# Kernel optimization log

Hardware: AMD Instinct MI355X
Metric: run time of the kernel (lower is better)

Reference implementation:

```python
import jax, jax.numpy as jnp
import numpy as np

D_MODEL, KAN_HIDDEN, NUM, K = 1024, 128, 3, 3  # grid_size=3, spline order k=3
GRID_RANGE = (-1.0, 1.0)


def make_grid(in_dim):
    # extended grid: num+1 interior knots padded by k steps of h on each side -> num+1+2k points
    h = (GRID_RANGE[1] - GRID_RANGE[0]) / NUM
    g = jnp.arange(-K, NUM + K + 1, dtype=jnp.float32) * h + GRID_RANGE[0]  # [num+1+2k]
    return jnp.broadcast_to(g, (in_dim, g.shape[0]))  # [in_dim, G]


def b_splines(x, grid):
    # Cox-de-Boor recursion. x: [N, D], grid: [D, G] -> basis [N, D, G-1-K]
    xg = x[:, :, None]  # [N, D, 1]
    B = ((xg >= grid[None, :, :-1]) & (xg < grid[None, :, 1:])).astype(x.dtype)
    for d in range(1, K + 1):
        left = (xg - grid[None, :, : -(d + 1)]) / (grid[:, d:-1] - grid[:, : -(d + 1)])[None]
        right = (grid[None, :, d + 1:] - xg) / (grid[:, d + 1:] - grid[:, 1:-d])[None]
        B = left * B[:, :, :-1] + right * B[:, :, 1:]
    return B  # [N, D, NUM+K]


def kan_layer(x, grid, coef, scale_base, scale_sp):
    # y[n,i,o] = scale_base[i,o]*silu(x[n,i]) + scale_sp[i,o]*sum_g B[n,i,g]*coef[i,o,g]; out = y.sum(i)
    B = b_splines(x, grid)  # [N, in, NUM+K]
    spline = jnp.einsum('nig,iog->no', B, coef * scale_sp[:, :, None])
    base = jnp.einsum('ni,io->no', jax.nn.silu(x), scale_base)
    return base + spline  # [N, out]


def setup_inputs() -> dict:
    key = jax.random.key(0)
    ks = jax.random.split(key, 7)
    s = 0.1  # small init scale for spline coefficients, matching noisy init spirit
    return {
        'x': jax.random.normal(ks[0], (4, 4096, D_MODEL), dtype=jnp.float32),
        'coef1': jax.random.normal(ks[1], (D_MODEL, KAN_HIDDEN, NUM + K), dtype=jnp.float32) * s,
        'scale_base1': jax.random.normal(ks[2], (D_MODEL, KAN_HIDDEN), dtype=jnp.float32),
        'scale_sp1': jnp.ones((D_MODEL, KAN_HIDDEN), dtype=jnp.float32),
        'coef2': jax.random.normal(ks[3], (KAN_HIDDEN, D_MODEL, NUM + K), dtype=jnp.float32) * s,
        'scale_base2': jax.random.normal(ks[4], (KAN_HIDDEN, D_MODEL), dtype=jnp.float32),
        'scale_sp2': jnp.ones((KAN_HIDDEN, D_MODEL), dtype=jnp.float32),
    }


def reference(x, coef1, scale_base1, scale_sp1, coef2, scale_base2, scale_sp2):
    b, s, d = x.shape
    xf = x.reshape(-1, d)  # [N, d_model]
    g1 = make_grid(D_MODEL)
    g2 = make_grid(KAN_HIDDEN)
    y1 = kan_layer(xf, g1, coef1, scale_base1, scale_sp1)   # [N, kan_hidden]
    y2 = kan_layer(y1, g2, coef2, scale_base2, scale_sp2)   # [N, d_model]
    return y2.reshape(b, s, d)
```

## Files before the change

### kernel.cpp

```cpp
#include <hip/hip_runtime.h>
#include <stdint.h>

typedef float f32x4 __attribute__((ext_vector_type(4)));
typedef __bf16 bf16x8 __attribute__((ext_vector_type(8)));

#define NROW 16384
#define DM   1024
#define HID  128
#define K1   8192
#define K2   1024

__device__ __forceinline__ unsigned short f2bf(float f) {
  unsigned u = __builtin_bit_cast(unsigned, f);
  u += 0x7fffu + ((u >> 16) & 1u);
  return (unsigned short)(u >> 16);
}

__device__ __forceinline__ uint32_t pkbf(float lo, float hi) {
  return (uint32_t)f2bf(lo) | ((uint32_t)f2bf(hi) << 16);
}

__device__ __forceinline__ void g2l16(const void* g, void* l) {
  __builtin_amdgcn_global_load_lds(
      (const __attribute__((address_space(1))) unsigned int*)g,
      (__attribute__((address_space(3))) unsigned int*)l, 16, 0, 0);
}

__device__ __forceinline__ bf16x8 expand8(float v) {
  const float t = (v + 3.0f) * 1.5f;
  const float cf = floorf(t);
  const float u = t - cf;
  int c = (int)cf;
  c = c < -1 ? -1 : c;
  c = c > 9 ? 9 : c;
  const float u2 = u * u, u3 = u2 * u, omu = 1.0f - u;
  const float p0 = u3 * (1.0f / 6.0f);
  const float p1 = (1.0f / 6.0f) + 0.5f * u + 0.5f * u2 - 0.5f * u3;
  const float p2 = (4.0f / 6.0f) - u2 + 0.5f * u3;
  const float p3 = omu * omu * omu * (1.0f / 6.0f);
  const uint64_t W = (uint64_t)pkbf(p3, p2) | ((uint64_t)pkbf(p1, p0) << 32);
  const int sa = (c - 2) * 16;
  const int sl = sa & 63;
  const uint64_t t1 = W << sl;
  const uint64_t t2 = (W >> (63 - sl)) >> 1;
  const uint64_t t3 = W >> ((-sa) & 63);
  const uint64_t L = sa < 0 ? t3 : (sa < 64 ? t1 : 0);
  const uint64_t H = sa < 0 ? 0  : (sa < 64 ? t2 : t1);
  const float s = v * __frcp_rn(1.0f + __expf(-v));
  const unsigned short sh = f2bf(s);
  const float shf = __builtin_bit_cast(float, (uint32_t)sh << 16);
  const unsigned short slo = f2bf(s - shf);
  const uint32_t w0 = ((uint32_t)L & 0xffff0000u) | sh;
  const uint32_t w1 = (uint32_t)(L >> 32);
  const uint32_t w2 = (uint32_t)H;
  const uint32_t w3 = ((uint32_t)(H >> 32) & 0xffffu) | ((uint32_t)slo << 16);
  union { uint4 q; bf16x8 b; } r;
  r.q = (uint4){w0, w1, w2, w3};
  return r.b;
}

__global__ void kan_prep_w1(const float* __restrict__ c1, const float* __restrict__ sb1,
                            const float* __restrict__ sp1, unsigned short* __restrict__ w1t) {
  const int t = blockIdx.x * 256 + threadIdx.x;
  const int o = t >> 10, i = t & 1023;
  const float sb = sb1[i * HID + o], sp = sp1[i * HID + o];
  const float* cf = c1 + (size_t)(i * HID + o) * 6;
  union { uint4 u; unsigned short h[8]; } r;
  const unsigned short b = f2bf(sb);
  r.h[0] = b; r.h[7] = b;
#pragma unroll
  for (int g = 0; g < 6; ++g) r.h[g + 1] = f2bf(cf[g] * sp);
  *(uint4*)(w1t + (size_t)o * K1 + i * 8) = r.u;
}

__global__ void kan_prep_w2(const float* __restrict__ c2, const float* __restrict__ sb2,
                            const float* __restrict__ sp2, unsigned short* __restrict__ w2t) {
  const int t = blockIdx.x * 256 + threadIdx.x;
  const int o = t >> 7, i = t & 127;
  const float sb = sb2[i * DM + o], sp = sp2[i * DM + o];
  const float* cf = c2 + (size_t)(i * DM + o) * 6;
  union { uint4 u; unsigned short h[8]; } r;
  const unsigned short b = f2bf(sb);
  r.h[0] = b; r.h[7] = b;
#pragma unroll
  for (int g = 0; g < 6; ++g) r.h[g + 1] = f2bf(cf[g] * sp);
  *(uint4*)(w2t + (size_t)o * K2 + i * 8) = r.u;
}

__global__ __launch_bounds__(512, 2) void kan_gemm1(
    const float* __restrict__ x, const unsigned short* __restrict__ w1t,
    float* __restrict__ yp) {
  __shared__ __align__(16) char lds[65536];
  const int tid = threadIdx.x;
  const int lane = tid & 63, w = tid >> 6;
  const int wk = w >> 2, wm = (w >> 1) & 1, wn = w & 1;
  const int mt = blockIdx.x >> 1, kh = blockIdx.x & 1;
  const int m0 = mt * 128;
  const int arow = tid >> 2, acs = (tid & 3) * 2;

  f32x4 acc[4][4];
#pragma unroll
  for (int a = 0; a < 4; ++a)
#pragma unroll
    for (int b = 0; b < 4; ++b) acc[a][b] = (f32x4){0.f, 0.f, 0.f, 0.f};

  const int bo = wn * 64 + (lane & 15);
  const int bk = wk * 32 + (lane >> 4) * 8;

  auto loadB = [&](int kt, bf16x8* bfrag) {
#pragma unroll
    for (int ni = 0; ni < 4; ++ni)
      bfrag[ni] = *(const bf16x8*)(w1t + (size_t)(bo + ni * 16) * K1 + kh * 4096 + kt * 64 + bk);
  };
  auto stageA = [&](float2 xv, int buf) {
    bf16x8 u0 = expand8(xv.x);
    bf16x8 u1 = expand8(xv.y);
    char* base = lds + buf * 16384;
    const int sw = (arow & 7) << 4;
    *(bf16x8*)(base + ((arow * 128 + acs * 16) ^ sw)) = u0;
    *(bf16x8*)(base + ((arow * 128 + acs * 16 + 16) ^ sw)) = u1;
  };

  const float* xrow = x + (size_t)(m0 + arow) * DM + kh * 512 + acs;
  bf16x8 bcur[4], bnxt[4];
  float2 xv = *(const float2*)xrow;
  loadB(0, bcur);
  stageA(xv, 0);
  xv = *(const float2*)(xrow + 8);
  __syncthreads();

  const int NT = 64;
  for (int kt = 0; kt < NT; ++kt) {
    const int cur = kt & 1;
    if (kt + 1 < NT) {
      loadB(kt + 1, bnxt);
      stageA(xv, cur ^ 1);
      if (kt + 2 < NT) xv = *(const float2*)(xrow + (kt + 2) * 8);
    }
    const char* ab = lds + cur * 16384;
    bf16x8 af[4];
#pragma unroll
    for (int mi = 0; mi < 4; ++mi) {
      const int row = wm * 64 + mi * 16 + (lane & 15);
      af[mi] = *(const bf16x8*)(ab + ((row * 128 + wk * 64 + (lane >> 4) * 16) ^ ((row & 7) << 4)));
    }
#pragma unroll
    for (int mi = 0; mi < 4; ++mi)
#pragma unroll
      for (int ni = 0; ni < 4; ++ni)
        acc[mi][ni] = __builtin_amdgcn_mfma_f32_16x16x32_bf16(af[mi], bcur[ni], acc[mi][ni], 0, 0, 0);
    __syncthreads();
#pragma unroll
    for (int ni = 0; ni < 4; ++ni) bcur[ni] = bnxt[ni];
  }

  if (wk == 1) {
    char* r = lds + (w & 3) * 16384;
#pragma unroll
    for (int mi = 0; mi < 4; ++mi)
#pragma unroll
      for (int ni = 0; ni < 4; ++ni)
        *(f32x4*)(r + (mi * 4 + ni) * 1024 + lane * 16) = acc[mi][ni];
  }
  __syncthreads();
  if (wk == 0) {
    const char* r = lds + w * 16384;
    float* yb = yp + (size_t)kh * NROW * HID;
#pragma unroll
    for (int mi = 0; mi < 4; ++mi)
#pragma unroll
      for (int ni = 0; ni < 4; ++ni) {
        f32x4 o = *(const f32x4*)(r + (mi * 4 + ni) * 1024 + lane * 16);
        o += acc[mi][ni];
        const int col = wn * 64 + ni * 16 + (lane & 15);
#pragma unroll
        for (int rr = 0; rr < 4; ++rr) {
          const int row = wm * 64 + mi * 16 + (lane >> 4) * 4 + rr;
          yb[(size_t)(m0 + row) * HID + col] = o[rr];
        }
      }
  }
}

__global__ void kan_combine(const float* __restrict__ yp, unsigned short* __restrict__ a2) {
  const size_t i = (size_t)blockIdx.x * 256 + threadIdx.x;
  const float v = yp[i] + yp[i + (size_t)NROW * HID];
  bf16x8 u = expand8(v);
  *(bf16x8*)(a2 + i * 8) = u;
}

__global__ __launch_bounds__(256, 2) void kan_gemm2(
    const unsigned short* __restrict__ a2, const unsigned short* __restrict__ w2t,
    float* __restrict__ out) {
  __shared__ __align__(16) unsigned short lds[2 * 16384];
  const int tid = threadIdx.x;
  const int lane = tid & 63, w = tid >> 6;
  const int wm = w >> 1, wn = w & 1;
  const int mt = blockIdx.x & 127, nt = blockIdx.x >> 7;
  const int m0 = mt * 128, n0 = nt * 128;

  f32x4 acc[4][4];
#pragma unroll
  for (int a = 0; a < 4; ++a)
#pragma unroll
    for (int b = 0; b < 4; ++b) acc[a][b] = (f32x4){0.f, 0.f, 0.f, 0.f};

  auto stage = [&](int kt, int buf) {
#pragma unroll
    for (int q = 0; q < 4; ++q) {
      const int r = (w * 4 + q) * 8 + (lane >> 3);
      const int slot = (lane & 7) ^ (lane >> 3);
      g2l16(a2 + (size_t)(m0 + r) * K2 + kt * 64 + slot * 8,
            (char*)lds + buf * 32768 + (w * 4 + q) * 1024);
      g2l16(w2t + (size_t)(n0 + r) * K2 + kt * 64 + slot * 8,
            (char*)lds + buf * 32768 + 16384 + (w * 4 + q) * 1024);
    }
  };

  stage(0, 0);
  __syncthreads();
  for (int kt = 0; kt < 16; ++kt) {
    const int cur = kt & 1;
    if (kt + 1 < 16) stage(kt + 1, cur ^ 1);
    const char* ab = (const char*)lds + cur * 32768;
    const char* bb = ab + 16384;
#pragma unroll
    for (int ks = 0; ks < 2; ++ks) {
      bf16x8 af[4], bfr[4];
#pragma unroll
      for (int mi = 0; mi < 4; ++mi) {
        const int row = wm * 64 + mi * 16 + (lane & 15);
        af[mi] = *(const bf16x8*)(ab + ((row * 128 + ks * 64 + (lane >> 4) * 16) ^ ((row & 7) << 4)));
      }
#pragma unroll
      for (int ni = 0; ni < 4; ++ni) {
        const int col = wn * 64 + ni * 16 + (lane & 15);
        bfr[ni] = *(const bf16x8*)(bb + ((col * 128 + ks * 64 + (lane >> 4) * 16) ^ ((col & 7) << 4)));
      }
#pragma unroll
      for (int mi = 0; mi < 4; ++mi)
#pragma unroll
        for (int ni = 0; ni < 4; ++ni)
          acc[mi][ni] = __builtin_amdgcn_mfma_f32_16x16x32_bf16(af[mi], bfr[ni], acc[mi][ni], 0, 0, 0);
    }
    __syncthreads();
  }

#pragma unroll
  for (int mi = 0; mi < 4; ++mi)
#pragma unroll
    for (int r = 0; r < 4; ++r) {
      const int row = wm * 64 + mi * 16 + (lane >> 4) * 4 + r;
#pragma unroll
      for (int ni = 0; ni < 4; ++ni) {
        const int col = wn * 64 + ni * 16 + (lane & 15);
        out[(size_t)(m0 + row) * DM + n0 + col] = acc[mi][ni][r];
      }
    }
}

extern "C" void kernel_launch(void* const* d_in, const int* in_sizes, int n_in,
                              void* d_out, int out_size, void* d_ws, size_t ws_size,
                              hipStream_t stream) {
  const float* x   = (const float*)d_in[0];
  const float* c1  = (const float*)d_in[1];
  const float* sb1 = (const float*)d_in[2];
  const float* sp1 = (const float*)d_in[3];
  const float* c2  = (const float*)d_in[4];
  const float* sb2 = (const float*)d_in[5];
  const float* sp2 = (const float*)d_in[6];
  float* out = (float*)d_out;

  unsigned short* w1t = (unsigned short*)d_ws;
  unsigned short* w2t = w1t + (size_t)HID * K1;
  unsigned short* a2  = w2t + (size_t)DM * K2;
  float*          yp  = (float*)(a2 + (size_t)NROW * K2);

  kan_prep_w1<<<512, 256, 0, stream>>>(c1, sb1, sp1, w1t);
  kan_prep_w2<<<512, 256, 0, stream>>>(c2, sb2, sp2, w2t);
  kan_gemm1<<<256, 512, 0, stream>>>(x, w1t, yp);
  kan_combine<<<NROW * HID / 256, 256, 0, stream>>>(yp, a2);
  kan_gemm2<<<(NROW / 128) * (DM / 128), 256, 0, stream>>>(a2, w2t, out);
}
```

Measured before the change: 130.5 us.

## Split GEMM1 K four ways with bf16 partials and halve its LDS footprint

GEMM1 now splits K across four blocks instead of two, giving 512 blocks and raising the occupancy target to 4 by halving LDS to 32KB. The cross-wave reduction moves to a two-round LDS exchange. Partial sums are written as bf16, which the combine kernel sums four at a time per thread. B fragments are loaded directly each iteration without double buffering. The spline and SiLU math uses FMAs and hardware conversion/rcp, and GEMM2 replaces syncthreads with explicit vmcnt waits plus raw barriers so the next tile's loads can overlap. The bf16 partial sums reduce precision in the intermediate activations, and the direct B loads may expose more global-load latency.

Result: slower. 135.7 us (+4.0%).

```diff
diff --git a/kernel.cpp b/kernel.cpp
--- a/kernel.cpp
+++ b/kernel.cpp
@@ -3,12 +3,15 @@
 
 typedef float f32x4 __attribute__((ext_vector_type(4)));
 typedef __bf16 bf16x8 __attribute__((ext_vector_type(8)));
+typedef __bf16 bf16x2 __attribute__((ext_vector_type(2)));
+typedef unsigned short ushort4v __attribute__((ext_vector_type(4)));
 
 #define NROW 16384
 #define DM   1024
 #define HID  128
 #define K1   8192
 #define K2   1024
+#define KSPLIT 4
 
 __device__ __forceinline__ unsigned short f2bf(float f) {
   unsigned u = __builtin_bit_cast(unsigned, f);
@@ -16,8 +19,11 @@
   return (unsigned short)(u >> 16);
 }
 
-__device__ __forceinline__ uint32_t pkbf(float lo, float hi) {
-  return (uint32_t)f2bf(lo) | ((uint32_t)f2bf(hi) << 16);
+__device__ __forceinline__ uint32_t pk2(float lo, float hi) {
+  bf16x2 v;
+  v[0] = (__bf16)lo;
+  v[1] = (__bf16)hi;
+  return __builtin_bit_cast(uint32_t, v);
 }
 
 __device__ __forceinline__ void g2l16(const void* g, void* l) {
@@ -35,10 +41,13 @@
   c = c > 9 ? 9 : c;
   const float u2 = u * u, u3 = u2 * u, omu = 1.0f - u;
   const float p0 = u3 * (1.0f / 6.0f);
-  const float p1 = (1.0f / 6.0f) + 0.5f * u + 0.5f * u2 - 0.5f * u3;
-  const float p2 = (4.0f / 6.0f) - u2 + 0.5f * u3;
-  const float p3 = omu * omu * omu * (1.0f / 6.0f);
-  const uint64_t W = (uint64_t)pkbf(p3, p2) | ((uint64_t)pkbf(p1, p0) << 32);
+  float p1 = __builtin_fmaf(0.5f, u, 1.0f / 6.0f);
+  p1 = __builtin_fmaf(0.5f, u2, p1);
+  p1 = __builtin_fmaf(-0.5f, u3, p1);
+  float p2 = __builtin_fmaf(0.5f, u3, 4.0f / 6.0f);
+  p2 = p2 - u2;
+  const float p3 = (omu * omu) * (omu * (1.0f / 6.0f));
+  const uint64_t W = (uint64_t)pk2(p3, p2) | ((uint64_t)pk2(p1, p0) << 32);
   const int sa = (c - 2) * 16;
   const int sl = sa & 63;
   const uint64_t t1 = W << sl;
@@ -46,14 +55,16 @@
   const uint64_t t3 = W >> ((-sa) & 63);
   const uint64_t L = sa < 0 ? t3 : (sa < 64 ? t1 : 0);
   const uint64_t H = sa < 0 ? 0  : (sa < 64 ? t2 : t1);
-  const float s = v * __frcp_rn(1.0f + __expf(-v));
-  const unsigned short sh = f2bf(s);
-  const float shf = __builtin_bit_cast(float, (uint32_t)sh << 16);
-  const unsigned short slo = f2bf(s - shf);
-  const uint32_t w0 = ((uint32_t)L & 0xffff0000u) | sh;
+  const float e = __expf(-v);
+  const float s = v * __builtin_amdgcn_rcpf(1.0f + e);
+  const uint32_t su = __builtin_bit_cast(uint32_t, s);
+  const uint32_t shf_bits = su & 0xffff0000u;
+  const float slo_f = s - __builtin_bit_cast(float, shf_bits);
+  const uint32_t slo = (uint32_t)__builtin_bit_cast(unsigned short, (__bf16)slo_f);
+  const uint32_t w0 = ((uint32_t)L & 0xffff0000u) | (shf_bits >> 16);
   const uint32_t w1 = (uint32_t)(L >> 32);
   const uint32_t w2 = (uint32_t)H;
-  const uint32_t w3 = ((uint32_t)(H >> 32) & 0xffffu) | ((uint32_t)slo << 16);
+  const uint32_t w3 = ((uint32_t)(H >> 32) & 0xffffu) | (slo << 16);
   union { uint4 q; bf16x8 b; } r;
   r.q = (uint4){w0, w1, w2, w3};
   return r.b;
@@ -87,14 +98,14 @@
   *(uint4*)(w2t + (size_t)o * K2 + i * 8) = r.u;
 }
 
-__global__ __launch_bounds__(512, 2) void kan_gemm1(
+__global__ __launch_bounds__(512, 4) void kan_gemm1(
     const float* __restrict__ x, const unsigned short* __restrict__ w1t,
-    float* __restrict__ yp) {
-  __shared__ __align__(16) char lds[65536];
+    unsigned short* __restrict__ yq) {
+  __shared__ __align__(16) char lds[32768];
   const int tid = threadIdx.x;
   const int lane = tid & 63, w = tid >> 6;
   const int wk = w >> 2, wm = (w >> 1) & 1, wn = w & 1;
-  const int mt = blockIdx.x >> 1, kh = blockIdx.x & 1;
+  const int mt = blockIdx.x >> 2, kh = blockIdx.x & 3;
   const int m0 = mt * 128;
   const int arow = tid >> 2, acs = (tid & 3) * 2;
 
@@ -105,88 +116,100 @@
     for (int b = 0; b < 4; ++b) acc[a][b] = (f32x4){0.f, 0.f, 0.f, 0.f};
 
   const int bo = wn * 64 + (lane & 15);
-  const int bk = wk * 32 + (lane >> 4) * 8;
-
-  auto loadB = [&](int kt, bf16x8* bfrag) {
-#pragma unroll
-    for (int ni = 0; ni < 4; ++ni)
-      bfrag[ni] = *(const bf16x8*)(w1t + (size_t)(bo + ni * 16) * K1 + kh * 4096 + kt * 64 + bk);
-  };
-  auto stageA = [&](float2 xv, int buf) {
-    bf16x8 u0 = expand8(xv.x);
-    bf16x8 u1 = expand8(xv.y);
-    char* base = lds + buf * 16384;
-    const int sw = (arow & 7) << 4;
-    *(bf16x8*)(base + ((arow * 128 + acs * 16) ^ sw)) = u0;
-    *(bf16x8*)(base + ((arow * 128 + acs * 16 + 16) ^ sw)) = u1;
-  };
-
-  const float* xrow = x + (size_t)(m0 + arow) * DM + kh * 512 + acs;
-  bf16x8 bcur[4], bnxt[4];
-  float2 xv = *(const float2*)xrow;
-  loadB(0, bcur);
-  stageA(xv, 0);
-  xv = *(const float2*)(xrow + 8);
+  const unsigned short* bp = w1t + (size_t)bo * K1 + kh * 2048 + wk * 32 + (lane >> 4) * 8;
+
+  const int wraw = arow * 128 + acs * 16;
+  const int wsw = (arow & 7) << 4;
+  char* wa0 = lds + (wraw ^ wsw);
+  char* wa1 = lds + ((wraw + 16) ^ wsw);
+  const char* ra[4];
+#pragma unroll
+  for (int mi = 0; mi < 4; ++mi) {
+    const int row = wm * 64 + mi * 16 + (lane & 15);
+    ra[mi] = lds + ((row * 128 + wk * 64 + (lane >> 4) * 16) ^ ((row & 7) << 4));
+  }
+  const float* xrow = x + (size_t)(m0 + arow) * DM + kh * 256 + acs;
+
+  bf16x8 b[4], af[4];
+  const int NT = 32;
+
+  {
+    float2 xv0 = *(const float2*)xrow;
+    *(bf16x8*)wa0 = expand8(xv0.x);
+    *(bf16x8*)wa1 = expand8(xv0.y);
+  }
+  float2 xv = *(const float2*)(xrow + 8);
   __syncthreads();
 
-  const int NT = 64;
   for (int kt = 0; kt < NT; ++kt) {
     const int cur = kt & 1;
+#pragma unroll
+    for (int ni = 0; ni < 4; ++ni)
+      b[ni] = *(const bf16x8*)(bp + (size_t)ni * 16 * K1 + kt * 64);
     if (kt + 1 < NT) {
-      loadB(kt + 1, bnxt);
-      stageA(xv, cur ^ 1);
-      if (kt + 2 < NT) xv = *(const float2*)(xrow + (kt + 2) * 8);
-    }
-    const char* ab = lds + cur * 16384;
-    bf16x8 af[4];
-#pragma unroll
-    for (int mi = 0; mi < 4; ++mi) {
-      const int row = wm * 64 + mi * 16 + (lane & 15);
-      af[mi] = *(const bf16x8*)(ab + ((row * 128 + wk * 64 + (lane >> 4) * 16) ^ ((row & 7) << 4)));
+      const int nb = (cur ^ 1) * 16384;
+      *(bf16x8*)(wa0 + nb) = expand8(xv.x);
+      *(bf16x8*)(wa1 + nb) = expand8(xv.y);
+      xv = *(const float2*)(xrow + ((kt + 2 < NT) ? kt + 2 : NT - 1) * 8);
     }
 #pragma unroll
     for (int mi = 0; mi < 4; ++mi)
+      af[mi] = *(const bf16x8*)(ra[mi] + cur * 16384);
+#pragma unroll
+    for (int mi = 0; mi < 4; ++mi)
 #pragma unroll
       for (int ni = 0; ni < 4; ++ni)
-        acc[mi][ni] = __builtin_amdgcn_mfma_f32_16x16x32_bf16(af[mi], bcur[ni], acc[mi][ni], 0, 0, 0);
+        acc[mi][ni] = __builtin_amdgcn_mfma_f32_16x16x32_bf16(af[mi], b[ni], acc[mi][ni], 0, 0, 0);
     __syncthreads();
-#pragma unroll
-    for (int ni = 0; ni < 4; ++ni) bcur[ni] = bnxt[ni];
-  }
-
-  if (wk == 1) {
-    char* r = lds + (w & 3) * 16384;
-#pragma unroll
-    for (int mi = 0; mi < 4; ++mi)
-#pragma unroll
-      for (int ni = 0; ni < 4; ++ni)
-        *(f32x4*)(r + (mi * 4 + ni) * 1024 + lane * 16) = acc[mi][ni];
-  }
-  __syncthreads();
-  if (wk == 0) {
-    const char* r = lds + w * 16384;
-    float* yb = yp + (size_t)kh * NROW * HID;
-#pragma unroll
-    for (int mi = 0; mi < 4; ++mi)
-#pragma unroll
-      for (int ni = 0; ni < 4; ++ni) {
-        f32x4 o = *(const f32x4*)(r + (mi * 4 + ni) * 1024 + lane * 16);
-        o += acc[mi][ni];
-        const int col = wn * 64 + ni * 16 + (lane & 15);
-#pragma unroll
-        for (int rr = 0; rr < 4; ++rr) {
-          const int row = wm * 64 + mi * 16 + (lane >> 4) * 4 + rr;
-          yb[(size_t)(m0 + row) * HID + col] = o[rr];
+  }
+
+  unsigned short* yb = yq + (size_t)kh * NROW * HID;
+#pragma unroll
+  for (int rnd = 0; rnd < 2; ++rnd) {
+    const int src0 = 4 + rnd * 2;
+    if (w == src0 || w == src0 + 1) {
+      char* r = lds + (w - src0) * 16384;
+#pragma unroll
+      for (int mi = 0; mi < 4; ++mi)
+#pragma unroll
+        for (int ni = 0; ni < 4; ++ni)
+          *(f32x4*)(r + (mi * 4 + ni) * 1024 + lane * 16) = acc[mi][ni];
+    }
+    __syncthreads();
+    const int snk0 = rnd * 2;
+    if (w == snk0 || w == snk0 + 1) {
+      const char* r = lds + (w - snk0) * 16384;
+#pragma unroll
+      for (int mi = 0; mi < 4; ++mi)
+#pragma unroll
+        for (int ni = 0; ni < 4; ++ni) {
+          f32x4 o = *(const f32x4*)(r + (mi * 4 + ni) * 1024 + lane * 16);
+          o += acc[mi][ni];
+          const int col = wn * 64 + ni * 16 + (lane & 15);
+#pragma unroll
+          for (int rr = 0; rr < 4; ++rr) {
+            const int row = wm * 64 + mi * 16 + (lane >> 4) * 4 + rr;
+            yb[(size_t)(m0 + row) * HID + col] = __builtin_bit_cast(unsigned short, (__bf16)o[rr]);
+          }
         }
-      }
-  }
-}
-
-__global__ void kan_combine(const float* __restrict__ yp, unsigned short* __restrict__ a2) {
-  const size_t i = (size_t)blockIdx.x * 256 + threadIdx.x;
-  const float v = yp[i] + yp[i + (size_t)NROW * HID];
-  bf16x8 u = expand8(v);
-  *(bf16x8*)(a2 + i * 8) = u;
+    }
+    __syncthreads();
+  }
+}
+
+__global__ void kan_combine(const unsigned short* __restrict__ yq, unsigned short* __restrict__ a2) {
+  const size_t i4 = ((size_t)blockIdx.x * 256 + threadIdx.x) * 4;
+  float v[4] = {0.f, 0.f, 0.f, 0.f};
+#pragma unroll
+  for (int h = 0; h < KSPLIT; ++h) {
+    ushort4v q = *(const ushort4v*)(yq + (size_t)h * NROW * HID + i4);
+#pragma unroll
+    for (int j = 0; j < 4; ++j)
+      v[j] += __builtin_bit_cast(float, (uint32_t)q[j] << 16);
+  }
+#pragma unroll
+  for (int j = 0; j < 4; ++j)
+    *(bf16x8*)(a2 + (i4 + j) * 8) = expand8(v[j]);
 }
 
 __global__ __launch_bounds__(256, 2) void kan_gemm2(
@@ -218,10 +241,16 @@
   };
 
   stage(0, 0);
-  __syncthreads();
   for (int kt = 0; kt < 16; ++kt) {
     const int cur = kt & 1;
-    if (kt + 1 < 16) stage(kt + 1, cur ^ 1);
+    if (kt + 1 < 16) {
+      stage(kt + 1, cur ^ 1);
+      asm volatile("s_waitcnt vmcnt(8)" ::: "memory");
+    } else {
+      asm volatile("s_waitcnt vmcnt(0)" ::: "memory");
+    }
+    __builtin_amdgcn_sched_barrier(0);
+    __builtin_amdgcn_s_barrier();
     const char* ab = (const char*)lds + cur * 32768;
     const char* bb = ab + 16384;
 #pragma unroll
@@ -243,7 +272,7 @@
         for (int ni = 0; ni < 4; ++ni)
           acc[mi][ni] = __builtin_amdgcn_mfma_f32_16x16x32_bf16(af[mi], bfr[ni], acc[mi][ni], 0, 0, 0);
     }
-    __syncthreads();
+    __builtin_amdgcn_s_barrier();
   }
 
 #pragma unroll
@@ -274,11 +303,11 @@
   unsigned short* w1t = (unsigned short*)d_ws;
   unsigned short* w2t = w1t + (size_t)HID * K1;
   unsigned short* a2  = w2t + (size_t)DM * K2;
-  float*          yp  = (float*)(a2 + (size_t)NROW * K2);
+  unsigned short* yq  = a2 + (size_t)NROW * K2;
 
   kan_prep_w1<<<512, 256, 0, stream>>>(c1, sb1, sp1, w1t);
   kan_prep_w2<<<512, 256, 0, stream>>>(c2, sb2, sp2, w2t);
-  kan_gemm1<<<256, 512, 0, stream>>>(x, w1t, yp);
-  kan_combine<<<NROW * HID / 256, 256, 0, stream>>>(yp, a2);
+  kan_gemm1<<<512, 512, 0, stream>>>(x, w1t, yq);
+  kan_combine<<<NROW * HID / 1024, 256, 0, stream>>>(yq, a2);
   kan_gemm2<<<(NROW / 128) * (DM / 128), 256, 0, stream>>>(a2, w2t, out);
 }
```
